# Kernel optimization log

Hardware: AMD Instinct MI355X
Metric: run time of the kernel (lower is better)

Reference implementation:

```python
import jax, jax.numpy as jnp
import numpy as np

EMBED_DIM = 1024
NUM_HEADS = 16
HEAD_DIM = EMBED_DIM // NUM_HEADS


def setup_inputs() -> dict:
    key = jax.random.key(0)
    ks = jax.random.split(key, 11)
    B, T, C = 2, 2048, EMBED_DIM
    s = 1.0 / np.sqrt(C)  # ~ torch Linear init scale
    inp = {
        "q": jax.random.normal(ks[0], (B, T, C), jnp.float32),
        "k": jax.random.normal(ks[1], (B, T, C), jnp.float32),
        "v": jax.random.normal(ks[2], (B, T, C), jnp.float32),
        "Wq": jax.random.normal(ks[3], (C, C), jnp.float32) * s,
        "bq": jax.random.normal(ks[4], (C,), jnp.float32) * s,
        "Wk": jax.random.normal(ks[5], (C, C), jnp.float32) * s,
        "bk": jax.random.normal(ks[6], (C,), jnp.float32) * s,
        "Wv": jax.random.normal(ks[7], (C, C), jnp.float32) * s,
        "bv": jax.random.normal(ks[8], (C,), jnp.float32) * s,
        "Wo": jax.random.normal(ks[9], (C, C), jnp.float32) * s,
        "bo": jax.random.normal(ks[10], (C,), jnp.float32) * s,
    }
    return inp


def _split_heads(x):
    B, T, C = x.shape
    return x.reshape(B, T, NUM_HEADS, HEAD_DIM).transpose(0, 2, 1, 3)  # [B,H,T,Dh]


def reference(q, k, v, Wq, bq, Wk, bk, Wv, bv, Wo, bo):
    B, Tq, C = q.shape
    # torch Linear: y = x @ W.T + b
    qh = _split_heads(q @ Wq.T + bq)
    kh = _split_heads(k @ Wk.T + bk)
    vh = _split_heads(v @ Wv.T + bv)
    scale = 1.0 / np.sqrt(HEAD_DIM).astype(np.float32)
    logits = jnp.einsum("bhqd,bhkd->bhqk", qh, kh) * scale
    attn = jax.nn.softmax(logits, axis=-1)
    out = jnp.einsum("bhqk,bhkd->bhqd", attn, vh)
    out = out.transpose(0, 2, 1, 3).reshape(B, Tq, C)
    return out @ Wo.T + bo
```

## Files before the change

kernel.cpp:

```cpp
#include <hip/hip_runtime.h>
#include <stdint.h>

#define T_SEQ 2048
#define CDIM 1024
#define NHEAD 16
#define HDIM 64
#define MROWS 4096

typedef unsigned short u16;
typedef __attribute__((ext_vector_type(8))) short bf16x8;
typedef __attribute__((ext_vector_type(4))) float f32x4;
typedef __attribute__((ext_vector_type(4))) unsigned short u16x4;

#if __has_builtin(__builtin_amdgcn_exp2f)
#define EXP2(x) __builtin_amdgcn_exp2f(x)
#else
#define EXP2(x) exp2f(x)
#endif

__device__ __forceinline__ u16 f2bf(float f) {
  unsigned u = __builtin_bit_cast(unsigned, f);
  u += 0x7fffu + ((u >> 16) & 1u);
  return (u16)(u >> 16);
}

__device__ __forceinline__ unsigned cvt_pk_bf16(float lo, float hi) {
  unsigned r;
  asm("v_cvt_pk_bf16_f32 %0, %1, %2" : "=v"(r) : "v"(lo), "v"(hi));
  return r;
}

__device__ __forceinline__ void gll16(const void* g, void* l) {
  __builtin_amdgcn_global_load_lds((__attribute__((address_space(1))) void*)(g),
                                   (__attribute__((address_space(3))) void*)(l),
                                   16, 0, 0);
}

__device__ __forceinline__ void wg_barrier() {
  asm volatile("" ::: "memory");
  __builtin_amdgcn_s_barrier();
  asm volatile("" ::: "memory");
}

#define WAIT_VM(N) do { __builtin_amdgcn_s_waitcnt(0xF00 | 0x70 | (N)); \
                        asm volatile("" ::: "memory"); } while (0)

__global__ __launch_bounds__(256)
void cvt_all(const float* __restrict__ q, const float* __restrict__ k, const float* __restrict__ v,
             const float* __restrict__ wq, const float* __restrict__ wk,
             const float* __restrict__ wv, const float* __restrict__ wo,
             u16* __restrict__ qb, u16* __restrict__ kb, u16* __restrict__ vb,
             u16* __restrict__ wqb, u16* __restrict__ wkb, u16* __restrict__ wvb, u16* __restrict__ wob) {
  int b = blockIdx.x;
  const float* src; u16* dst; int base;
  if (b < 1536) {
    int s = b >> 9;
    src = (s == 0) ? q : (s == 1) ? k : v;
    dst = (s == 0) ? qb : (s == 1) ? kb : vb;
    base = (b & 511) * 2048;
  } else {
    int s = (b - 1536) >> 7;
    src = (s == 0) ? wq : (s == 1) ? wk : (s == 2) ? wv : wo;
    dst = (s == 0) ? wqb : (s == 1) ? wkb : (s == 2) ? wvb : wob;
    base = ((b - 1536) & 127) * 2048;
  }
#pragma unroll
  for (int j = 0; j < 8; ++j) {
    int i = base + j * 256 + threadIdx.x;
    float4 a = ((const float4*)src)[i];
    u16x4 o = { f2bf(a.x), f2bf(a.y), f2bf(a.z), f2bf(a.w) };
    ((u16x4*)dst)[i] = o;
  }
}


__device__ __forceinline__ void gemm_stage(const u16* Ag, const u16* Bg, u16* Ad, u16* Bd) {
#pragma unroll
  for (int c = 0; c < 4; ++c) {
    gll16(Ag + c * 32 * CDIM, Ad + c * 2048);
    gll16(Bg + c * 32 * CDIM, Bd + c * 2048);
  }
}

__device__ __forceinline__ void gemm_compute(const u16* As, const u16* Bs,
                                             f32x4 (&acc)[4][4],
                                             int wr, int wc, int lg, int lr) {
#pragma unroll
  for (int kk = 0; kk < 2; ++kk) {
    bf16x8 af[4], bfr[4];
#pragma unroll
    for (int f = 0; f < 4; ++f) {
      int ra = wr * 64 + f * 16 + lr;
      af[f]  = *(const bf16x8*)((const char*)As + ra * 128 + ((lg * 16 + kk * 64) ^ ((ra & 7) << 4)));
      int rb = wc * 64 + f * 16 + lr;
      bfr[f] = *(const bf16x8*)((const char*)Bs + rb * 128 + ((lg * 16 + kk * 64) ^ ((rb & 7) << 4)));
    }
#pragma unroll
    for (int i = 0; i < 4; ++i)
#pragma unroll
      for (int j = 0; j < 4; ++j)
        acc[i][j] = __builtin_amdgcn_mfma_f32_16x16x32_bf16(af[i], bfr[j], acc[i][j], 0, 0, 0);
  }
}

#define GEMM_KLOOP(As, Bs, Ad0, Bd0, Ad1, Bd1)                                 \
  gemm_stage(Ag, Bg, Ad0, Bd0);                                                \
  _Pragma("unroll 1")                                                          \
  for (int kt = 0; kt < 16; ++kt) {                                            \
    wg_barrier();                                                              \
    int nt = (kt + 1 < 16) ? kt + 1 : 15;                                      \
    if (kt & 1) gemm_stage(Ag + nt * 64, Bg + nt * 64, Ad0, Bd0);              \
    else        gemm_stage(Ag + nt * 64, Bg + nt * 64, Ad1, Bd1);              \
    WAIT_VM(8);                                                                \
    wg_barrier();                                                              \
    gemm_compute((kt & 1) ? As[1] : As[0], (kt & 1) ? Bs[1] : Bs[0],           \
                 acc, wr, wc, lg, lr);                                         \
  }

__global__ __launch_bounds__(256)
void gemm_qkv(const u16* __restrict__ A0, const u16* __restrict__ A1, const u16* __restrict__ A2,
              const u16* __restrict__ W0, const u16* __restrict__ W1, const u16* __restrict__ W2,
              const float* __restrict__ b0, const float* __restrict__ b1, const float* __restrict__ b2,
              u16* __restrict__ o0, u16* __restrict__ o1, u16* __restrict__ o2,
              float qscale) {
  __shared__ u16 As[2][128 * 64];
  __shared__ u16 Bs[2][128 * 64];
  const int z = blockIdx.z;
  const u16* A   = (z == 0) ? A0 : (z == 1) ? A1 : A2;
  const u16* Bw  = (z == 0) ? W0 : (z == 1) ? W1 : W2;
  const float* bias = (z == 0) ? b0 : (z == 1) ? b1 : b2;
  u16* outp = (z == 0) ? o0 : (z == 1) ? o1 : o2;
  const float scale = (z == 0) ? qscale : 1.0f;

  const int m0 = blockIdx.y * 128;
  const int n0 = blockIdx.x * 128;
  const int tid = threadIdx.x;
  const int w = tid >> 6, l = tid & 63;
  const int wr = w >> 1, wc = w & 1;
  const int lg = l >> 4, lr = l & 15;

  const int row0 = tid >> 3, slot0 = tid & 7;
  const int so = (slot0 ^ (row0 & 7)) << 3;
  const u16* Ag = A  + ((size_t)(m0 + row0)) * CDIM + so;
  const u16* Bg = Bw + ((size_t)(n0 + row0)) * CDIM + so;
  u16* Ad0 = As[0] + w * 512;  u16* Bd0 = Bs[0] + w * 512;
  u16* Ad1 = As[1] + w * 512;  u16* Bd1 = Bs[1] + w * 512;

  f32x4 acc[4][4] = {};

  GEMM_KLOOP(As, Bs, Ad0, Bd0, Ad1, Bd1)

#pragma unroll
  for (int fj = 0; fj < 4; ++fj) {
    int col = n0 + wc * 64 + fj * 16 + lr;
    float bv = bias[col];
    int h = col >> 6, d = col & 63;
#pragma unroll
    for (int fi = 0; fi < 4; ++fi) {
#pragma unroll
      for (int i = 0; i < 4; ++i) {
        int row = m0 + wr * 64 + fi * 16 + lg * 4 + i;
        float val = (acc[fi][fj][i] + bv) * scale;
        int b = row >> 11, t = row & 2047;
        if (z < 2)
          outp[(((size_t)(b * NHEAD + h)) * T_SEQ + t) * HDIM + d] = f2bf(val);
        else
          outp[(((size_t)(b * NHEAD + h)) * HDIM + d) * T_SEQ + t] = f2bf(val);
      }
    }
  }
}

__global__ __launch_bounds__(256)
void gemm_bt0(const u16* __restrict__ A, const u16* __restrict__ Bw,
              const float* __restrict__ bias, float* __restrict__ outp) {
  __shared__ u16 As[2][128 * 64];
  __shared__ u16 Bs[2][128 * 64];
  const int m0 = blockIdx.y * 128;
  const int n0 = blockIdx.x * 128;
  const int tid = threadIdx.x;
  const int w = tid >> 6, l = tid & 63;
  const int wr = w >> 1, wc = w & 1;
  const int lg = l >> 4, lr = l & 15;

  const int row0 = tid >> 3, slot0 = tid & 7;
  const int so = (slot0 ^ (row0 & 7)) << 3;
  const u16* Ag = A  + ((size_t)(m0 + row0)) * CDIM + so;
  const u16* Bg = Bw + ((size_t)(n0 + row0)) * CDIM + so;
  u16* Ad0 = As[0] + w * 512;  u16* Bd0 = Bs[0] + w * 512;
  u16* Ad1 = As[1] + w * 512;  u16* Bd1 = Bs[1] + w * 512;

  f32x4 acc[4][4] = {};

  GEMM_KLOOP(As, Bs, Ad0, Bd0, Ad1, Bd1)

#pragma unroll
  for (int fj = 0; fj < 4; ++fj) {
    int col = n0 + wc * 64 + fj * 16 + lr;
    float bv = bias[col];
#pragma unroll
    for (int fi = 0; fi < 4; ++fi) {
#pragma unroll
      for (int i = 0; i < 4; ++i) {
        int row = m0 + wr * 64 + fi * 16 + lg * 4 + i;
        outp[(size_t)row * CDIM + col] = acc[fi][fj][i] + bv;
      }
    }
  }
}


__device__ __forceinline__ void attn_stage(const u16* Kg, const u16* Vg, u16* Kd, u16* Vd) {
#pragma unroll
  for (int c = 0; c < 2; ++c) {
    gll16(Kg + c * 32 * HDIM,  Kd + c * 2048);
    gll16(Vg + c * 32 * T_SEQ, Vd + c * 2048);
  }
}

__device__ __forceinline__ void attn_process(const u16* Ks, const u16* Vs, u16* pw,
                                             bf16x8 qf0, bf16x8 qf1,
                                             f32x4 (&acc)[4], f32x4& lsum, float& m_run,
                                             int lg, int lr) {
  f32x4 s[4] = {};
  __builtin_amdgcn_s_setprio(1);
#pragma unroll
  for (int kk = 0; kk < 2; ++kk) {
    bf16x8 qf = kk ? qf1 : qf0;
#pragma unroll
    for (int fn = 0; fn < 4; ++fn) {
      int r = fn * 16 + lr;
      bf16x8 kf = *(const bf16x8*)((const char*)Ks + r * 128 + ((lg * 16 + kk * 64) ^ ((r & 7) << 4)));
      s[fn] = __builtin_amdgcn_mfma_f32_16x16x32_bf16(kf, qf, s[fn], 0, 0, 0);
    }
  }
  __builtin_amdgcn_s_setprio(0);

  float t0 = fmaxf(fmaxf(s[0][0], s[0][1]), fmaxf(s[0][2], s[0][3]));
  float t1 = fmaxf(fmaxf(s[1][0], s[1][1]), fmaxf(s[1][2], s[1][3]));
  float t2 = fmaxf(fmaxf(s[2][0], s[2][1]), fmaxf(s[2][2], s[2][3]));
  float t3 = fmaxf(fmaxf(s[3][0], s[3][1]), fmaxf(s[3][2], s[3][3]));
  float tl = fmaxf(fmaxf(t0, t1), fmaxf(t2, t3));
  if (!__all(tl <= m_run + 8.f)) {
    float tmax = fmaxf(tl, __shfl_xor(tl, 16));
    tmax = fmaxf(tmax, __shfl_xor(tmax, 32));
    float m_new = fmaxf(m_run, tmax);
    float alpha = EXP2(m_run - m_new);
    lsum[0] *= alpha; lsum[1] *= alpha; lsum[2] *= alpha; lsum[3] *= alpha;
#pragma unroll
    for (int fd = 0; fd < 4; ++fd) {
      acc[fd][0] *= alpha; acc[fd][1] *= alpha;
      acc[fd][2] *= alpha; acc[fd][3] *= alpha;
    }
    m_run = m_new;
  }

#pragma unroll
  for (int fn = 0; fn < 4; ++fn) {
    float p0 = EXP2(s[fn][0] - m_run);
    float p1 = EXP2(s[fn][1] - m_run);
    float p2 = EXP2(s[fn][2] - m_run);
    float p3 = EXP2(s[fn][3] - m_run);
    lsum[fn] += (p0 + p1) + (p2 + p3);
    uint2 pk;
    pk.x = cvt_pk_bf16(p0, p1);
    pk.y = cvt_pk_bf16(p2, p3);
    *(uint2*)((char*)pw + lr * 128 + ((fn * 32 + lg * 8) ^ ((lr & 7) << 4))) = pk;
  }

#pragma unroll
  for (int kk = 0; kk < 2; ++kk) {
    bf16x8 pf = *(const bf16x8*)((const char*)pw + lr * 128 + ((lg * 16 + kk * 64) ^ ((lr & 7) << 4)));
    __builtin_amdgcn_s_setprio(1);
#pragma unroll
    for (int fd = 0; fd < 4; ++fd) {
      int r = fd * 16 + lr;
      bf16x8 vf = *(const bf16x8*)((const char*)Vs + r * 128 + ((lg * 16 + kk * 64) ^ ((r & 7) << 4)));
      acc[fd] = __builtin_amdgcn_mfma_f32_16x16x32_bf16(vf, pf, acc[fd], 0, 0, 0);
    }
    __builtin_amdgcn_s_setprio(0);
  }
}

__global__ __launch_bounds__(256)
void attn_fused(const u16* __restrict__ Qh, const u16* __restrict__ Kh,
                const u16* __restrict__ Vt, u16* __restrict__ Ao) {
  __shared__ u16 Ks[2][64 * 64];
  __shared__ u16 Vs[2][64 * 64];
  __shared__ u16 Ps[4][16 * 64];
  const int bh = blockIdx.y;
  const int q0 = blockIdx.x * 64;
  const int tid = threadIdx.x;
  const int w = tid >> 6, l = tid & 63;
  const int lg = l >> 4, lr = l & 15;

  const u16* qptr = Qh + ((size_t)bh * T_SEQ + q0 + w * 16 + lr) * HDIM + lg * 8;
  bf16x8 qf0 = *(const bf16x8*)qptr;
  bf16x8 qf1 = *(const bf16x8*)(qptr + 32);

  const int row0 = tid >> 3, slot0 = tid & 7;
  const int so = (slot0 ^ (row0 & 7)) << 3;
  const u16* Kg = Kh + ((size_t)bh * T_SEQ + row0) * HDIM + so;
  const u16* Vg = Vt + ((size_t)bh * HDIM + row0) * T_SEQ + so;
  u16* Kd0 = Ks[0] + w * 512;  u16* Vd0 = Vs[0] + w * 512;
  u16* Kd1 = Ks[1] + w * 512;  u16* Vd1 = Vs[1] + w * 512;

  f32x4 acc[4] = {};
  f32x4 lsum = {};
  float m_run = -1e30f;
  u16* pw = Ps[w];

  attn_stage(Kg, Vg, Kd0, Vd0);
#pragma unroll 1
  for (int kv = 0; kv < 32; ++kv) {
    wg_barrier();
    int nt = (kv + 1 < 32) ? kv + 1 : 31;
    if (kv & 1) attn_stage(Kg + (size_t)nt * 64 * HDIM, Vg + nt * 64, Kd0, Vd0);
    else        attn_stage(Kg + (size_t)nt * 64 * HDIM, Vg + nt * 64, Kd1, Vd1);
    WAIT_VM(4);
    wg_barrier();
    attn_process((kv & 1) ? Ks[1] : Ks[0], (kv & 1) ? Vs[1] : Vs[0],
                 pw, qf0, qf1, acc, lsum, m_run, lg, lr);
  }

  float lr_sum = (lsum[0] + lsum[1]) + (lsum[2] + lsum[3]);
  lr_sum += __shfl_xor(lr_sum, 16);
  lr_sum += __shfl_xor(lr_sum, 32);
  float inv = 1.f / lr_sum;

  int b = bh >> 4, h = bh & 15;
  u16* orow = Ao + ((size_t)(b * T_SEQ + q0 + w * 16 + lr)) * CDIM + h * HDIM;
#pragma unroll
  for (int fd = 0; fd < 4; ++fd) {
    uint2 ov;
    ov.x = cvt_pk_bf16(acc[fd][0] * inv, acc[fd][1] * inv);
    ov.y = cvt_pk_bf16(acc[fd][2] * inv, acc[fd][3] * inv);
    *(uint2*)(orow + fd * 16 + lg * 4) = ov;
  }
}

extern "C" void kernel_launch(void* const* d_in, const int* in_sizes, int n_in,
                              void* d_out, int out_size, void* d_ws, size_t ws_size,
                              hipStream_t stream) {
  const float* q  = (const float*)d_in[0];
  const float* k  = (const float*)d_in[1];
  const float* v  = (const float*)d_in[2];
  const float* Wq = (const float*)d_in[3];
  const float* bq = (const float*)d_in[4];
  const float* Wk = (const float*)d_in[5];
  const float* bk = (const float*)d_in[6];
  const float* Wv = (const float*)d_in[7];
  const float* bv = (const float*)d_in[8];
  const float* Wo = (const float*)d_in[9];
  const float* bo = (const float*)d_in[10];

  char* ws = (char*)d_ws;
  size_t off = 0;
  auto alloc = [&](size_t n) { void* p = ws + off; off += (n + 255) & ~(size_t)255; return p; };
  const size_t NX = (size_t)MROWS * CDIM;
  const size_t NW = (size_t)CDIM * CDIM;
  u16* qb  = (u16*)alloc(NX * 2);
  u16* kb  = (u16*)alloc(NX * 2);
  u16* vb  = (u16*)alloc(NX * 2);
  u16* Wqb = (u16*)alloc(NW * 2);
  u16* Wkb = (u16*)alloc(NW * 2);
  u16* Wvb = (u16*)alloc(NW * 2);
  u16* Wob = (u16*)alloc(NW * 2);
  u16* Qhp = (u16*)alloc(NX * 2);
  u16* Khp = (u16*)alloc(NX * 2);
  u16* Vtp = (u16*)alloc(NX * 2);
  u16* Aop = (u16*)alloc(NX * 2);

  cvt_all<<<2048, 256, 0, stream>>>(q, k, v, Wq, Wk, Wv, Wo,
                                    qb, kb, vb, Wqb, Wkb, Wvb, Wob);

  const float qscale = 0.18033688011112042f;
  gemm_qkv<<<dim3(CDIM / 128, MROWS / 128, 3), 256, 0, stream>>>(
      qb, kb, vb, Wqb, Wkb, Wvb, bq, bk, bv, Qhp, Khp, Vtp, qscale);

  attn_fused<<<dim3(T_SEQ / 64, 32), 256, 0, stream>>>(Qhp, Khp, Vtp, Aop);

  gemm_bt0<<<dim3(CDIM / 128, MROWS / 128), 256, 0, stream>>>(Aop, Wob, bo, (float*)d_out);

  (void)in_sizes; (void)n_in; (void)out_size; (void)ws_size;
}
```

Before: 140.7 us.

## Switch attention to 32x32 MFMA with register P transpose and 128-query blocks

The attention kernel now uses 32x32x16 bf16 MFMAs, so each wave handles 32 queries and each block 128 queries, which halves the grid and doubles reuse of every K/V tile loaded into LDS. The softmax probabilities are rearranged into the PV operand layout in registers with v_permlane32_swap instead of a round trip through a per-wave LDS P buffer. The output is staged through LDS so each thread writes a 16-byte coalesced store. In exchange the grid has half as many blocks, which may lower occupancy, and per-thread register pressure goes up.

```diff
diff --git a/kernel.cpp b/kernel.cpp
--- a/kernel.cpp
+++ b/kernel.cpp
@@ -10,7 +10,9 @@
 typedef unsigned short u16;
 typedef __attribute__((ext_vector_type(8))) short bf16x8;
 typedef __attribute__((ext_vector_type(4))) float f32x4;
+typedef __attribute__((ext_vector_type(16))) float f32x16;
 typedef __attribute__((ext_vector_type(4))) unsigned short u16x4;
+typedef __attribute__((ext_vector_type(4))) unsigned int uint4v;
 
 #if __has_builtin(__builtin_amdgcn_exp2f)
 #define EXP2(x) __builtin_amdgcn_exp2f(x)
@@ -28,6 +30,10 @@
   unsigned r;
   asm("v_cvt_pk_bf16_f32 %0, %1, %2" : "=v"(r) : "v"(lo), "v"(hi));
   return r;
+}
+
+__device__ __forceinline__ void pls(unsigned &a, unsigned &b) {
+  asm("v_permlane32_swap_b32 %0, %1" : "+v"(a), "+v"(b));
 }
 
 __device__ __forceinline__ void gll16(const void* g, void* l) {
@@ -218,68 +224,70 @@
   }
 }
 
-__device__ __forceinline__ void attn_process(const u16* Ks, const u16* Vs, u16* pw,
-                                             bf16x8 qf0, bf16x8 qf1,
-                                             f32x4 (&acc)[4], f32x4& lsum, float& m_run,
-                                             int lg, int lr) {
-  f32x4 s[4] = {};
+__device__ __forceinline__ void attn_tile(const char* Kb, const char* Vb,
+                                          const bf16x8 (&qf)[4],
+                                          f32x16 (&acc)[2], f32x4& lsum, float& m_run,
+                                          int lo5, int hi, int swz) {
+  f32x16 s[2] = {};
+  const int colK = 16 * hi;
   __builtin_amdgcn_s_setprio(1);
 #pragma unroll
-  for (int kk = 0; kk < 2; ++kk) {
-    bf16x8 qf = kk ? qf1 : qf0;
-#pragma unroll
-    for (int fn = 0; fn < 4; ++fn) {
-      int r = fn * 16 + lr;
-      bf16x8 kf = *(const bf16x8*)((const char*)Ks + r * 128 + ((lg * 16 + kk * 64) ^ ((r & 7) << 4)));
-      s[fn] = __builtin_amdgcn_mfma_f32_16x16x32_bf16(kf, qf, s[fn], 0, 0, 0);
-    }
+  for (int st = 0; st < 4; ++st) {
+    bf16x8 k0 = *(const bf16x8*)(Kb + lo5 * 128        + ((32 * st + colK) ^ swz));
+    bf16x8 k1 = *(const bf16x8*)(Kb + (lo5 + 32) * 128 + ((32 * st + colK) ^ swz));
+    s[0] = __builtin_amdgcn_mfma_f32_32x32x16_bf16(k0, qf[st], s[0], 0, 0, 0);
+    s[1] = __builtin_amdgcn_mfma_f32_32x32x16_bf16(k1, qf[st], s[1], 0, 0, 0);
   }
   __builtin_amdgcn_s_setprio(0);
 
-  float t0 = fmaxf(fmaxf(s[0][0], s[0][1]), fmaxf(s[0][2], s[0][3]));
-  float t1 = fmaxf(fmaxf(s[1][0], s[1][1]), fmaxf(s[1][2], s[1][3]));
-  float t2 = fmaxf(fmaxf(s[2][0], s[2][1]), fmaxf(s[2][2], s[2][3]));
-  float t3 = fmaxf(fmaxf(s[3][0], s[3][1]), fmaxf(s[3][2], s[3][3]));
-  float tl = fmaxf(fmaxf(t0, t1), fmaxf(t2, t3));
+  float t[8];
+#pragma unroll
+  for (int i = 0; i < 8; ++i)
+    t[i] = fmaxf(fmaxf(s[0][2 * i], s[0][2 * i + 1]), fmaxf(s[1][2 * i], s[1][2 * i + 1]));
+  float u0 = fmaxf(fmaxf(t[0], t[1]), fmaxf(t[2], t[3]));
+  float u1 = fmaxf(fmaxf(t[4], t[5]), fmaxf(t[6], t[7]));
+  float tl = fmaxf(u0, u1);
   if (!__all(tl <= m_run + 8.f)) {
-    float tmax = fmaxf(tl, __shfl_xor(tl, 16));
-    tmax = fmaxf(tmax, __shfl_xor(tmax, 32));
+    float tmax = fmaxf(tl, __shfl_xor(tl, 32));
     float m_new = fmaxf(m_run, tmax);
     float alpha = EXP2(m_run - m_new);
     lsum[0] *= alpha; lsum[1] *= alpha; lsum[2] *= alpha; lsum[3] *= alpha;
 #pragma unroll
-    for (int fd = 0; fd < 4; ++fd) {
-      acc[fd][0] *= alpha; acc[fd][1] *= alpha;
-      acc[fd][2] *= alpha; acc[fd][3] *= alpha;
+    for (int i = 0; i < 16; ++i) { acc[0][i] *= alpha; acc[1][i] *= alpha; }
+    m_run = m_new;
+  }
+
+  unsigned pg[2][8];
+#pragma unroll
+  for (int g = 0; g < 8; ++g) {
+    float a0 = EXP2(s[0][2 * g] - m_run), b0 = EXP2(s[0][2 * g + 1] - m_run);
+    float a1 = EXP2(s[1][2 * g] - m_run), b1 = EXP2(s[1][2 * g + 1] - m_run);
+    lsum[g & 3] += (a0 + b0) + (a1 + b1);
+    pg[0][g] = cvt_pk_bf16(a0, b0);
+    pg[1][g] = cvt_pk_bf16(a1, b1);
+  }
+
+  bf16x8 pb[4];
+#pragma unroll
+  for (int sub = 0; sub < 2; ++sub)
+#pragma unroll
+    for (int ks = 0; ks < 2; ++ks) {
+      unsigned w0 = pg[sub][4 * ks + 0], w1 = pg[sub][4 * ks + 1];
+      unsigned w2 = pg[sub][4 * ks + 2], w3 = pg[sub][4 * ks + 3];
+      pls(w0, w2); pls(w1, w3);
+      uint4v tt = { w0, w1, w2, w3 };
+      pb[2 * sub + ks] = __builtin_bit_cast(bf16x8, tt);
     }
-    m_run = m_new;
-  }
-
-#pragma unroll
-  for (int fn = 0; fn < 4; ++fn) {
-    float p0 = EXP2(s[fn][0] - m_run);
-    float p1 = EXP2(s[fn][1] - m_run);
-    float p2 = EXP2(s[fn][2] - m_run);
-    float p3 = EXP2(s[fn][3] - m_run);
-    lsum[fn] += (p0 + p1) + (p2 + p3);
-    uint2 pk;
-    pk.x = cvt_pk_bf16(p0, p1);
-    pk.y = cvt_pk_bf16(p2, p3);
-    *(uint2*)((char*)pw + lr * 128 + ((fn * 32 + lg * 8) ^ ((lr & 7) << 4))) = pk;
-  }
-
-#pragma unroll
-  for (int kk = 0; kk < 2; ++kk) {
-    bf16x8 pf = *(const bf16x8*)((const char*)pw + lr * 128 + ((lg * 16 + kk * 64) ^ ((lr & 7) << 4)));
-    __builtin_amdgcn_s_setprio(1);
-#pragma unroll
-    for (int fd = 0; fd < 4; ++fd) {
-      int r = fd * 16 + lr;
-      bf16x8 vf = *(const bf16x8*)((const char*)Vs + r * 128 + ((lg * 16 + kk * 64) ^ ((r & 7) << 4)));
-      acc[fd] = __builtin_amdgcn_mfma_f32_16x16x32_bf16(vf, pf, acc[fd], 0, 0, 0);
-    }
-    __builtin_amdgcn_s_setprio(0);
-  }
+
+  __builtin_amdgcn_s_setprio(1);
+#pragma unroll
+  for (int ks = 0; ks < 4; ++ks) {
+    bf16x8 v0 = *(const bf16x8*)(Vb + lo5 * 128        + ((32 * ks + colK) ^ swz));
+    bf16x8 v1 = *(const bf16x8*)(Vb + (lo5 + 32) * 128 + ((32 * ks + colK) ^ swz));
+    acc[0] = __builtin_amdgcn_mfma_f32_32x32x16_bf16(v0, pb[ks], acc[0], 0, 0, 0);
+    acc[1] = __builtin_amdgcn_mfma_f32_32x32x16_bf16(v1, pb[ks], acc[1], 0, 0, 0);
+  }
+  __builtin_amdgcn_s_setprio(0);
 }
 
 __global__ __launch_bounds__(256)
@@ -287,16 +295,17 @@
                 const u16* __restrict__ Vt, u16* __restrict__ Ao) {
   __shared__ u16 Ks[2][64 * 64];
   __shared__ u16 Vs[2][64 * 64];
-  __shared__ u16 Ps[4][16 * 64];
   const int bh = blockIdx.y;
-  const int q0 = blockIdx.x * 64;
+  const int q0 = blockIdx.x * 128;
   const int tid = threadIdx.x;
   const int w = tid >> 6, l = tid & 63;
-  const int lg = l >> 4, lr = l & 15;
-
-  const u16* qptr = Qh + ((size_t)bh * T_SEQ + q0 + w * 16 + lr) * HDIM + lg * 8;
-  bf16x8 qf0 = *(const bf16x8*)qptr;
-  bf16x8 qf1 = *(const bf16x8*)(qptr + 32);
+  const int lo5 = l & 31, hi = l >> 5;
+  const int swz = (l & 7) << 4;
+
+  const u16* qptr = Qh + ((size_t)bh * T_SEQ + q0 + w * 32 + lo5) * HDIM + hi * 8;
+  bf16x8 qf[4];
+#pragma unroll
+  for (int s = 0; s < 4; ++s) qf[s] = *(const bf16x8*)(qptr + 16 * s);
 
   const int row0 = tid >> 3, slot0 = tid & 7;
   const int so = (slot0 ^ (row0 & 7)) << 3;
@@ -305,10 +314,9 @@
   u16* Kd0 = Ks[0] + w * 512;  u16* Vd0 = Vs[0] + w * 512;
   u16* Kd1 = Ks[1] + w * 512;  u16* Vd1 = Vs[1] + w * 512;
 
-  f32x4 acc[4] = {};
+  f32x16 acc[2] = {};
   f32x4 lsum = {};
   float m_run = -1e30f;
-  u16* pw = Ps[w];
 
   attn_stage(Kg, Vg, Kd0, Vd0);
 #pragma unroll 1
@@ -319,23 +327,33 @@
     else        attn_stage(Kg + (size_t)nt * 64 * HDIM, Vg + nt * 64, Kd1, Vd1);
     WAIT_VM(4);
     wg_barrier();
-    attn_process((kv & 1) ? Ks[1] : Ks[0], (kv & 1) ? Vs[1] : Vs[0],
-                 pw, qf0, qf1, acc, lsum, m_run, lg, lr);
-  }
-
-  float lr_sum = (lsum[0] + lsum[1]) + (lsum[2] + lsum[3]);
-  lr_sum += __shfl_xor(lr_sum, 16);
-  lr_sum += __shfl_xor(lr_sum, 32);
-  float inv = 1.f / lr_sum;
-
+    attn_tile((const char*)(kv & 1 ? Ks[1] : Ks[0]),
+              (const char*)(kv & 1 ? Vs[1] : Vs[0]),
+              qf, acc, lsum, m_run, lo5, hi, swz);
+  }
+
+  float ls = (lsum[0] + lsum[1]) + (lsum[2] + lsum[3]);
+  ls += __shfl_xor(ls, 32);
+  float inv = 1.f / ls;
+
+  wg_barrier();
+  char* os = (char*)(Ks[0]) + w * 4096;
+#pragma unroll
+  for (int dsub = 0; dsub < 2; ++dsub)
+#pragma unroll
+    for (int gg = 0; gg < 4; ++gg) {
+      unsigned wa = cvt_pk_bf16(acc[dsub][4 * gg + 0] * inv, acc[dsub][4 * gg + 1] * inv);
+      unsigned wb = cvt_pk_bf16(acc[dsub][4 * gg + 2] * inv, acc[dsub][4 * gg + 3] * inv);
+      uint2 wv = { wa, wb };
+      int byte = lo5 * 128 + (((32 * dsub + 8 * gg + 4 * hi) * 2) ^ swz);
+      *(uint2*)(os + byte) = wv;
+    }
   int b = bh >> 4, h = bh & 15;
-  u16* orow = Ao + ((size_t)(b * T_SEQ + q0 + w * 16 + lr)) * CDIM + h * HDIM;
-#pragma unroll
-  for (int fd = 0; fd < 4; ++fd) {
-    uint2 ov;
-    ov.x = cvt_pk_bf16(acc[fd][0] * inv, acc[fd][1] * inv);
-    ov.y = cvt_pk_bf16(acc[fd][2] * inv, acc[fd][3] * inv);
-    *(uint2*)(orow + fd * 16 + lg * 4) = ov;
+#pragma unroll
+  for (int c = 0; c < 4; ++c) {
+    int qq = 8 * c + (l >> 3);
+    uint4v ov = *(const uint4v*)(os + qq * 128 + ((16 * (l & 7)) ^ ((qq & 7) << 4)));
+    *(uint4v*)(Ao + ((size_t)(b * T_SEQ + q0 + w * 32 + qq)) * CDIM + h * HDIM + (l & 7) * 8) = ov;
   }
 }
 
@@ -378,7 +396,7 @@
   gemm_qkv<<<dim3(CDIM / 128, MROWS / 128, 3), 256, 0, stream>>>(
       qb, kb, vb, Wqb, Wkb, Wvb, bq, bk, bv, Qhp, Khp, Vtp, qscale);
 
-  attn_fused<<<dim3(T_SEQ / 64, 32), 256, 0, stream>>>(Qhp, Khp, Vtp, Aop);
+  attn_fused<<<dim3(T_SEQ / 128, 32), 256, 0, stream>>>(Qhp, Khp, Vtp, Aop);
 
   gemm_bt0<<<dim3(CDIM / 128, MROWS / 128), 256, 0, stream>>>(Aop, Wob, bo, (float*)d_out);
 
```

Measured after the change: 136.0 us. 1.03x faster.
